# Performance work log

Hardware: AMD Instinct MI355X
Metric: run time of the kernel (lower is better)

The kernel has to match this reference:

```python
import jax, jax.numpy as jnp
import numpy as np

N_NODES = 50000
N_EDGES = 800000
N_GRAPHS = 500
DIM = 64          # node feature dim
NG = 64           # num gaussians (edge rbf dim)
CUTOFF = 12.0
NCONV = 3
HID = 128
NTYPES = 100      # atom vocabulary for embedding
EPS = 1e-5        # batchnorm eps


def _bn(x, g, b):
    # training-mode batchnorm over the leading (edge/node) axis
    m = jnp.mean(x, axis=0)
    v = jnp.var(x, axis=0)
    return g * (x - m) * jax.lax.rsqrt(v + EPS) + b


def setup_inputs() -> dict:
    key = jax.random.key(0)
    ks = jax.random.split(key, 12)
    atom_types = jax.random.randint(ks[0], (N_NODES,), 0, NTYPES)
    src = jax.random.randint(ks[1], (N_EDGES,), 0, N_NODES)
    dst = jax.random.randint(ks[2], (N_EDGES,), 0, N_NODES)
    graph_ids = jnp.sort(jax.random.randint(ks[3], (N_NODES,), 0, N_GRAPHS))
    distance = jax.random.uniform(ks[4], (N_EDGES,), dtype=jnp.float32) * CUTOFF
    cin = 2 * DIM + NG
    s = 0.05
    embed_table = jax.random.normal(ks[5], (NTYPES, DIM), dtype=jnp.float32) * s
    W1 = jax.random.normal(ks[6], (NCONV, cin, DIM), dtype=jnp.float32) * s
    b1 = jnp.zeros((NCONV, DIM), jnp.float32)
    W2 = jax.random.normal(ks[7], (NCONV, cin, DIM), dtype=jnp.float32) * s
    b2 = jnp.zeros((NCONV, DIM), jnp.float32)
    g1 = jnp.ones((NCONV, DIM), jnp.float32); bt1 = jnp.zeros((NCONV, DIM), jnp.float32)
    g2 = jnp.ones((NCONV, DIM), jnp.float32); bt2 = jnp.zeros((NCONV, DIM), jnp.float32)
    g3 = jnp.ones((NCONV, DIM), jnp.float32); bt3 = jnp.zeros((NCONV, DIM), jnp.float32)
    Wfc = jax.random.normal(ks[8], (DIM, HID), dtype=jnp.float32) * s
    bfc = jnp.zeros((HID,), jnp.float32)
    Wout = jax.random.normal(ks[9], (HID, 1), dtype=jnp.float32) * s
    bout = jnp.zeros((1,), jnp.float32)
    return dict(atom_types=atom_types, src=src, dst=dst, graph_ids=graph_ids,
                distance=distance, embed_table=embed_table,
                W1=W1, b1=b1, W2=W2, b2=b2,
                g1=g1, bt1=bt1, g2=g2, bt2=bt2, g3=g3, bt3=bt3,
                Wfc=Wfc, bfc=bfc, Wout=Wout, bout=bout)


def reference(atom_types, src, dst, graph_ids, distance, embed_table,
              W1, b1, W2, b2, g1, bt1, g2, bt2, g3, bt3,
              Wfc, bfc, Wout, bout):
    # embedding lookup
    node = embed_table[atom_types]                           # [N, DIM]
    # RBF expansion of distances (gaussian smearing on [0, CUTOFF])
    mu = jnp.linspace(0.0, CUTOFF, NG, dtype=jnp.float32)
    coeff = -0.5 / (mu[1] - mu[0]) ** 2
    rbf = jnp.exp(coeff * (distance[:, None] - mu) ** 2)      # [E, NG]

    for i in range(NCONV):
        # gather: concat(src feats, dst feats, edge rbf)
        te = jnp.concatenate([node[src], node[dst], rbf], axis=-1)  # [E, 192]
        nbr_filter = jax.nn.sigmoid(_bn(te @ W1[i] + b1[i], g1[i], bt1[i]))
        # NOTE: faithful to the source bug: bn2 is applied to nbr_filter,
        # so fc_full2 (W2/b2) output is computed in torch but unused.
        nbr_core = jax.nn.softplus(_bn(nbr_filter, g2[i], bt2[i]))
        h = nbr_filter * nbr_core                              # [E, DIM]
        # scatter-sum messages to destination nodes
        agg = jax.ops.segment_sum(h, dst, num_segments=N_NODES)
        node = node + _bn(agg, g3[i], bt3[i])

    # avg pooling per graph
    sums = jax.ops.segment_sum(node, graph_ids, num_segments=N_GRAPHS)
    cnts = jax.ops.segment_sum(jnp.ones((N_NODES, 1), node.dtype), graph_ids,
                               num_segments=N_GRAPHS)
    crys = sums / jnp.maximum(cnts, 1.0)                       # [G, DIM]

    crys = jax.nn.softplus(crys) @ Wfc + bfc
    crys = jax.nn.softplus(crys)
    return crys @ Wout + bout                                  # [G, 1]
```

## Files before the change

kernel.cpp:

```cpp
#include <hip/hip_runtime.h>
#include <hip/hip_fp16.h>
#include <math.h>

#define DIM 64
#define NG 64
#define CIN 192
#define HID 128
#define NCONV 3
#define TB 2048
#define CUTOFF 12.0f
#define EPS 1e-5f
#define SCB 256

typedef int i2v __attribute__((ext_vector_type(2)));
typedef int i4v __attribute__((ext_vector_type(4)));

__device__ __forceinline__ float sp_(float y) {
    return fmaxf(y, 0.f) + __logf(1.f + __expf(-fabsf(y)));
}
__device__ __forceinline__ float sig_(float y) {
    return 1.f / (1.f + __expf(-y));
}
__device__ __forceinline__ float2 h2f2_bits(int bits) {
    __half2 h;
    __builtin_memcpy(&h, &bits, 4);
    return __half22float2(h);
}
__device__ __forceinline__ int f2h2_bits(float a, float b) {
    __half2 h;
    h.x = __float2half(a);
    h.y = __float2half(b);
    int r;
    __builtin_memcpy(&r, &h, 4);
    return r;
}

__global__ void k_tables(const float* __restrict__ W1, __half2* __restrict__ Tp) {
    int row = blockIdx.x;
    int l = row / TB, i = row % TB;
    int d = threadIdx.x;
    const float stepmu = CUTOFF / (float)(NG - 1);
    const float coeff = -0.5f / (stepmu * stepmu);
    const float stepx = CUTOFF / (float)(TB - 1);
    float x0 = (float)i * stepx;
    float x1 = fminf((float)(i + 1), (float)(TB - 1)) * stepx;
    __shared__ float r0[NG];
    __shared__ float r1[NG];
    float mu = (float)d * stepmu;
    float d0 = x0 - mu, d1 = x1 - mu;
    r0[d] = expf(coeff * d0 * d0);
    r1[d] = expf(coeff * d1 * d1);
    __syncthreads();
    const float* w = W1 + (size_t)(l * CIN + 2 * DIM) * DIM;
    float a0 = 0.f, a1 = 0.f;
#pragma unroll 8
    for (int g = 0; g < NG; ++g) {
        float wv = w[g * DIM + d];
        a0 += r0[g] * wv;
        a1 += r1[g] * wv;
    }
    __half2 hh;
    hh.x = __float2half(a0);
    hh.y = __float2half(a1);
    Tp[(size_t)row * DIM + d] = hh;
}

__global__ void k_hist(const int* __restrict__ dst, int* __restrict__ cnt, int E) {
    for (int e = blockIdx.x * blockDim.x + threadIdx.x; e < E;
         e += gridDim.x * blockDim.x)
        atomicAdd(&cnt[dst[e]], 1);
}

__global__ void k_scanA(const int* __restrict__ cnt, int* __restrict__ bsum, int N) {
    __shared__ int lds[SCB];
    int i = blockIdx.x * SCB + threadIdx.x;
    lds[threadIdx.x] = (i < N) ? cnt[i] : 0;
    __syncthreads();
    for (int o = SCB / 2; o > 0; o >>= 1) {
        if (threadIdx.x < o) lds[threadIdx.x] += lds[threadIdx.x + o];
        __syncthreads();
    }
    if (threadIdx.x == 0) bsum[blockIdx.x] = lds[0];
}

__global__ void k_scanB(const int* __restrict__ bsum, int* __restrict__ bexcl, int NB) {
    __shared__ int lds[SCB];
    int t = threadIdx.x;
    int v = (t < NB) ? bsum[t] : 0;
    lds[t] = v;
    __syncthreads();
    for (int o = 1; o < SCB; o <<= 1) {
        int add = (t >= o) ? lds[t - o] : 0;
        __syncthreads();
        lds[t] += add;
        __syncthreads();
    }
    if (t < NB) bexcl[t] = lds[t] - v;
}

__global__ void k_scanC(const int* __restrict__ cnt, const int* __restrict__ bexcl,
                        int* __restrict__ off, int* __restrict__ cursor, int N, int E) {
    __shared__ int lds[SCB];
    int t = threadIdx.x;
    int i = blockIdx.x * SCB + t;
    int v = (i < N) ? cnt[i] : 0;
    lds[t] = v;
    __syncthreads();
    for (int o = 1; o < SCB; o <<= 1) {
        int add = (t >= o) ? lds[t - o] : 0;
        __syncthreads();
        lds[t] += add;
        __syncthreads();
    }
    if (i < N) {
        int excl = bexcl[blockIdx.x] + lds[t] - v;
        off[i] = excl;
        cursor[i] = excl;
        if (i == N - 1) off[N] = E;
    }
}

__global__ void k_scatter(const int* __restrict__ src, const int* __restrict__ dst,
                          const float* __restrict__ dist, int* __restrict__ cursor,
                          int2* __restrict__ es, int E) {
    const float inv_step = (float)(TB - 1) / CUTOFF;
    for (int e = blockIdx.x * blockDim.x + threadIdx.x; e < E;
         e += gridDim.x * blockDim.x) {
        int t = dst[e];
        int pos = atomicAdd(&cursor[t], 1);
        es[pos] = make_int2(src[e], __float_as_int(dist[e] * inv_step));
    }
}

template <int FIRST>
__global__ void __launch_bounds__(256) k_pq(
        const int* __restrict__ at, const float* __restrict__ emb,
        float* __restrict__ node, const float* __restrict__ agg,
        const double* __restrict__ st, const float* __restrict__ g3,
        const float* __restrict__ bt3, double invN,
        const float* __restrict__ W1, const float* __restrict__ b1, int l,
        __half* __restrict__ P16, float* __restrict__ Q, int N) {
    __shared__ float wa[DIM * DIM];
    __shared__ float wb[DIM * DIM];
    const float* WA = W1 + (size_t)(l * CIN) * DIM;
    for (int k = threadIdx.x; k < DIM * DIM; k += blockDim.x) {
        wa[k] = WA[k];
        wb[k] = WA[DIM * DIM + k];
    }
    int lane = threadIdx.x & 63, w = threadIdx.x >> 6;
    float bv = b1[lane];
    float a3 = 0.f, c3 = 0.f;
    if (!FIRST) {
        double m = st[lane] * invN;
        double v = st[64 + lane] * invN - m * m;
        a3 = g3[lane] / sqrtf((float)v + EPS);
        c3 = bt3[lane] - a3 * (float)m;
    }
    __syncthreads();
    int wpb = blockDim.x >> 6;
    for (int n = blockIdx.x * wpb + w; n < N; n += gridDim.x * wpb) {
        float nv;
        if (FIRST) {
            nv = emb[at[n] * DIM + lane];
        } else {
            nv = node[n * DIM + lane] + a3 * agg[n * DIM + lane] + c3;
        }
        node[n * DIM + lane] = nv;
        float ap = 0.f, aq = bv;
#pragma unroll 8
        for (int k = 0; k < DIM; ++k) {
            float b = __shfl(nv, k);
            ap += b * wa[k * DIM + lane];
            aq += b * wb[k * DIM + lane];
        }
        P16[n * DIM + lane] = __float2half(ap);
        Q[n * DIM + lane] = aq;
    }
}

__global__ void __launch_bounds__(256) k_convA(
        const int* __restrict__ off, const int2* __restrict__ es,
        const __half* __restrict__ P16, const float* __restrict__ Q,
        const __half2* __restrict__ Tp,
        double* __restrict__ stats, __half* __restrict__ z16, int N) {
    int lane = threadIdx.x & 63;
    int w = threadIdx.x >> 6;
    int dg = lane & 15;
    int slot = lane >> 4;
    int d0 = dg * 4;
    float s00 = 0.f, s01 = 0.f, s02 = 0.f, s03 = 0.f;
    float s10 = 0.f, s11 = 0.f, s12 = 0.f, s13 = 0.f;
    int gw = blockIdx.x * 4 + w, nw = gridDim.x * 4;
    for (int n = gw; n < N; n += nw) {
        int e0 = off[n], e1 = off[n + 1];
        if (e0 >= e1) continue;
        float4 q4 = *(const float4*)(Q + (size_t)n * DIM + d0);
        for (int eb = e0; eb < e1; eb += 8) {
            int eA = eb + slot, eB = eA + 4;
            bool vA = (eA < e1), vB = (eB < e1);
            int2 evA = es[vA ? eA : e1 - 1];
            int2 evB = es[vB ? eB : e1 - 1];
            float uA = __int_as_float(evA.y), uB = __int_as_float(evB.y);
            int iA = (int)uA, iB = (int)uB;
            iA = max(0, min(iA, TB - 2));
            iB = max(0, min(iB, TB - 2));
            float frA = uA - (float)iA, frB = uB - (float)iB;
            i2v pbA = *(const i2v*)(P16 + (size_t)evA.x * DIM + d0);
            i2v pbB = *(const i2v*)(P16 + (size_t)evB.x * DIM + d0);
            i4v tbA = *(const i4v*)(Tp + (size_t)iA * DIM + d0);
            i4v tbB = *(const i4v*)(Tp + (size_t)iB * DIM + d0);
            {
                float2 p01 = h2f2_bits(pbA.x), p23 = h2f2_bits(pbA.y);
                float2 t0 = h2f2_bits(tbA.x), t1 = h2f2_bits(tbA.y);
                float2 t2 = h2f2_bits(tbA.z), t3 = h2f2_bits(tbA.w);
                float z0 = p01.x + t0.x + frA * (t0.y - t0.x) + q4.x;
                float z1 = p01.y + t1.x + frA * (t1.y - t1.x) + q4.y;
                float z2 = p23.x + t2.x + frA * (t2.y - t2.x) + q4.z;
                float z3 = p23.y + t3.x + frA * (t3.y - t3.x) + q4.w;
                if (vA) {
                    i2v zz;
                    zz.x = f2h2_bits(z0, z1);
                    zz.y = f2h2_bits(z2, z3);
                    *(i2v*)(z16 + (size_t)eA * DIM + d0) = zz;
                    s00 += z0; s10 += z0 * z0;
                    s01 += z1; s11 += z1 * z1;
                    s02 += z2; s12 += z2 * z2;
                    s03 += z3; s13 += z3 * z3;
                }
            }
            {
                float2 p01 = h2f2_bits(pbB.x), p23 = h2f2_bits(pbB.y);
                float2 t0 = h2f2_bits(tbB.x), t1 = h2f2_bits(tbB.y);
                float2 t2 = h2f2_bits(tbB.z), t3 = h2f2_bits(tbB.w);
                float z0 = p01.x + t0.x + frB * (t0.y - t0.x) + q4.x;
                float z1 = p01.y + t1.x + frB * (t1.y - t1.x) + q4.y;
                float z2 = p23.x + t2.x + frB * (t2.y - t2.x) + q4.z;
                float z3 = p23.y + t3.x + frB * (t3.y - t3.x) + q4.w;
                if (vB) {
                    i2v zz;
                    zz.x = f2h2_bits(z0, z1);
                    zz.y = f2h2_bits(z2, z3);
                    *(i2v*)(z16 + (size_t)eB * DIM + d0) = zz;
                    s00 += z0; s10 += z0 * z0;
                    s01 += z1; s11 += z1 * z1;
                    s02 += z2; s12 += z2 * z2;
                    s03 += z3; s13 += z3 * z3;
                }
            }
        }
    }
    __shared__ float r0[4][64][4];
    __shared__ float r1[4][64][4];
    r0[w][lane][0] = s00; r0[w][lane][1] = s01;
    r0[w][lane][2] = s02; r0[w][lane][3] = s03;
    r1[w][lane][0] = s10; r1[w][lane][1] = s11;
    r1[w][lane][2] = s12; r1[w][lane][3] = s13;
    __syncthreads();
    if (threadIdx.x < 64) {
        int d = threadIdx.x;
        int dgg = d >> 2, q = d & 3;
        float t0 = 0.f, t1 = 0.f;
#pragma unroll
        for (int ww = 0; ww < 4; ++ww)
#pragma unroll
            for (int sl = 0; sl < 4; ++sl) {
                t0 += r0[ww][sl * 16 + dgg][q];
                t1 += r1[ww][sl * 16 + dgg][q];
            }
        atomicAdd(&stats[d], (double)t0);
        atomicAdd(&stats[64 + d], (double)t1);
    }
}

__global__ void __launch_bounds__(256) k_statsF(
        __half* __restrict__ zf16,
        const double* __restrict__ stA, const float* __restrict__ gA,
        const float* __restrict__ btA,
        double* __restrict__ stats, int total8, double invE) {
    int gq = threadIdx.x & 7;
    float a1[8], c1[8];
#pragma unroll
    for (int q = 0; q < 8; ++q) {
        int d = gq * 8 + q;
        double m = stA[d] * invE;
        double v = stA[64 + d] * invE - m * m;
        a1[q] = gA[d] / sqrtf((float)v + EPS);
        c1[q] = btA[d] - a1[q] * (float)m;
    }
    float s0[8] = {0, 0, 0, 0, 0, 0, 0, 0};
    float s1[8] = {0, 0, 0, 0, 0, 0, 0, 0};
    i4v* z4 = (i4v*)zf16;
    int tid = blockIdx.x * blockDim.x + threadIdx.x;
    int stride = gridDim.x * blockDim.x;
    for (int i = tid; i < total8; i += stride) {
        i4v v = z4[i];
        float2 p0 = h2f2_bits(v.x);
        float2 p1 = h2f2_bits(v.y);
        float2 p2 = h2f2_bits(v.z);
        float2 p3 = h2f2_bits(v.w);
        float f0 = sig_(a1[0] * p0.x + c1[0]);
        float f1 = sig_(a1[1] * p0.y + c1[1]);
        float f2 = sig_(a1[2] * p1.x + c1[2]);
        float f3 = sig_(a1[3] * p1.y + c1[3]);
        float f4 = sig_(a1[4] * p2.x + c1[4]);
        float f5 = sig_(a1[5] * p2.y + c1[5]);
        float f6 = sig_(a1[6] * p3.x + c1[6]);
        float f7 = sig_(a1[7] * p3.y + c1[7]);
        i4v o;
        o.x = f2h2_bits(f0, f1);
        o.y = f2h2_bits(f2, f3);
        o.z = f2h2_bits(f4, f5);
        o.w = f2h2_bits(f6, f7);
        z4[i] = o;
        s0[0] += f0; s1[0] += f0 * f0;
        s0[1] += f1; s1[1] += f1 * f1;
        s0[2] += f2; s1[2] += f2 * f2;
        s0[3] += f3; s1[3] += f3 * f3;
        s0[4] += f4; s1[4] += f4 * f4;
        s0[5] += f5; s1[5] += f5 * f5;
        s0[6] += f6; s1[6] += f6 * f6;
        s0[7] += f7; s1[7] += f7 * f7;
    }
    __shared__ float lds[256][16];
#pragma unroll
    for (int q = 0; q < 8; ++q) {
        lds[threadIdx.x][q] = s0[q];
        lds[threadIdx.x][8 + q] = s1[q];
    }
    __syncthreads();
    if (threadIdx.x < 64) {
        int d = threadIdx.x;
        int grp = d >> 3, j = d & 7;
        float t0 = 0.f, t1 = 0.f;
        for (int k = 0; k < 32; ++k) {
            int t = k * 8 + grp;
            t0 += lds[t][j];
            t1 += lds[t][8 + j];
        }
        atomicAdd(&stats[d], (double)t0);
        atomicAdd(&stats[64 + d], (double)t1);
    }
}

__global__ void __launch_bounds__(256) k_aggF(
        const int* __restrict__ off, const __half* __restrict__ f16,
        const double* __restrict__ stB, const float* __restrict__ gB,
        const float* __restrict__ btB,
        double* __restrict__ stats, float* __restrict__ agg, int N, double invE) {
    int lane = threadIdx.x & 63;
    int w = threadIdx.x >> 6;
    int dg = lane & 7;
    int slot = lane >> 3;
    int d0 = dg * 8;
    float a2[8], c2[8];
#pragma unroll
    for (int q = 0; q < 8; ++q) {
        int d = d0 + q;
        double m = stB[d] * invE, v = stB[64 + d] * invE - m * m;
        a2[q] = gB[d] / sqrtf((float)v + EPS);
        c2[q] = btB[d] - a2[q] * (float)m;
    }
    float s0[8] = {0, 0, 0, 0, 0, 0, 0, 0};
    float s1[8] = {0, 0, 0, 0, 0, 0, 0, 0};
    int gw = blockIdx.x * 4 + w, nw = gridDim.x * 4;
    for (int n = gw; n < N; n += nw) {
        int e0 = off[n], e1 = off[n + 1];
        float tot[8] = {0, 0, 0, 0, 0, 0, 0, 0};
        for (int eb = e0; eb < e1; eb += 16) {
            int eA = eb + slot, eB = eA + 8;
            float mkA = (eA < e1) ? 1.f : 0.f;
            float mkB = (eB < e1) ? 1.f : 0.f;
            int ecA = (eA < e1) ? eA : (e1 - 1);
            int ecB = (eB < e1) ? eB : (e1 - 1);
            i4v zbA = *(const i4v*)(f16 + (size_t)ecA * DIM + d0);
            i4v zbB = *(const i4v*)(f16 + (size_t)ecB * DIM + d0);
            float2 a0 = h2f2_bits(zbA.x), a1v = h2f2_bits(zbA.y);
            float2 a2v = h2f2_bits(zbA.z), a3v = h2f2_bits(zbA.w);
            float2 b0 = h2f2_bits(zbB.x), b1v = h2f2_bits(zbB.y);
            float2 b2v = h2f2_bits(zbB.z), b3v = h2f2_bits(zbB.w);
            float fA[8] = {a0.x, a0.y, a1v.x, a1v.y, a2v.x, a2v.y, a3v.x, a3v.y};
            float fB[8] = {b0.x, b0.y, b1v.x, b1v.y, b2v.x, b2v.y, b3v.x, b3v.y};
#pragma unroll
            for (int q = 0; q < 8; ++q) {
                float hA = fA[q] * sp_(a2[q] * fA[q] + c2[q]);
                float hB = fB[q] * sp_(a2[q] * fB[q] + c2[q]);
                tot[q] += mkA * hA + mkB * hB;
            }
        }
#pragma unroll
        for (int q = 0; q < 8; ++q) {
            float v = tot[q];
            v += __shfl_xor(v, 8);
            v += __shfl_xor(v, 16);
            v += __shfl_xor(v, 32);
            tot[q] = v;
        }
        if (slot == 0) {
            float4 w0 = make_float4(tot[0], tot[1], tot[2], tot[3]);
            float4 w1 = make_float4(tot[4], tot[5], tot[6], tot[7]);
            *(float4*)(agg + (size_t)n * DIM + d0) = w0;
            *(float4*)(agg + (size_t)n * DIM + d0 + 4) = w1;
#pragma unroll
            for (int q = 0; q < 8; ++q) {
                s0[q] += tot[q];
                s1[q] += tot[q] * tot[q];
            }
        }
    }
    __shared__ float r0[4][8][8];
    __shared__ float r1[4][8][8];
    if (slot == 0) {
#pragma unroll
        for (int q = 0; q < 8; ++q) {
            r0[w][dg][q] = s0[q];
            r1[w][dg][q] = s1[q];
        }
    }
    __syncthreads();
    if (threadIdx.x < 64) {
        int d = threadIdx.x;
        int dgg = d >> 3, q = d & 7;
        float t0 = 0.f, t1 = 0.f;
#pragma unroll
        for (int ww = 0; ww < 4; ++ww) {
            t0 += r0[ww][dgg][q];
            t1 += r1[ww][dgg][q];
        }
        atomicAdd(&stats[d], (double)t0);
        atomicAdd(&stats[64 + d], (double)t1);
    }
}

template <int MODE>
__global__ void __launch_bounds__(256) k_conv(
        const int* __restrict__ off, const int2* __restrict__ es,
        const __half* __restrict__ P16, const float* __restrict__ Q,
        const __half2* __restrict__ Tp,
        const double* __restrict__ stA, const float* __restrict__ gA,
        const float* __restrict__ btA,
        const double* __restrict__ stB, const float* __restrict__ gB,
        const float* __restrict__ btB,
        double* __restrict__ stats, float* __restrict__ agg, int N, double invE) {
    int lane = threadIdx.x & 63;
    int w = threadIdx.x >> 6;
    float a1 = 0.f, c1 = 0.f, a2 = 0.f, c2 = 0.f;
    if (MODE >= 2) {
        double m = stA[lane] * invE;
        double v = stA[64 + lane] * invE - m * m;
        a1 = gA[lane] / sqrtf((float)v + EPS);
        c1 = btA[lane] - a1 * (float)m;
    }
    if (MODE == 3) {
        double m = stB[lane] * invE;
        double v = stB[64 + lane] * invE - m * m;
        a2 = gB[lane] / sqrtf((float)v + EPS);
        c2 = btB[lane] - a2 * (float)m;
    }
    float s0 = 0.f, s1 = 0.f;
    int gw = blockIdx.x * 4 + w, nw = gridDim.x * 4;
    for (int n = gw; n < N; n += nw) {
        int e0 = off[n], e1 = off[n + 1];
        float qc = Q[n * DIM + lane];
        float acc = 0.f;
        auto body = [&](int2 ev) {
            float u = __int_as_float(ev.y);
            int i = (int)u;
            i = max(0, min(i, TB - 2));
            float fr = u - (float)i;
            float2 t2 = __half22float2(Tp[(size_t)i * DIM + lane]);
            float p = __half2float(P16[(size_t)ev.x * DIM + lane]);
            float z = p + t2.x + fr * (t2.y - t2.x) + qc;
            if (MODE == 0) { s0 += z; s1 += z * z; }
            else {
                float f = sig_(a1 * z + c1);
                if (MODE == 2) { s0 += f; s1 += f * f; }
                else acc += f * sp_(a2 * f + c2);
            }
        };
        int e = e0;
        for (; e + 2 <= e1; e += 2) { body(es[e]); body(es[e + 1]); }
        if (e < e1) body(es[e]);
        if (MODE == 3) {
            agg[n * DIM + lane] = acc;
            s0 += acc; s1 += acc * acc;
        }
    }
    __shared__ float r0[4][64];
    __shared__ float r1[4][64];
    r0[w][lane] = s0;
    r1[w][lane] = s1;
    __syncthreads();
    if (threadIdx.x < 64) {
        int d = threadIdx.x;
        float t0 = r0[0][d] + r0[1][d] + r0[2][d] + r0[3][d];
        float t1 = r1[0][d] + r1[1][d] + r1[2][d] + r1[3][d];
        atomicAdd(&stats[d], (double)t0);
        atomicAdd(&stats[64 + d], (double)t1);
    }
}

__global__ void k_head(const float* __restrict__ node, const float* __restrict__ agg,
                       const double* __restrict__ st, const float* __restrict__ g3,
                       const float* __restrict__ bt3, double invN,
                       const int* __restrict__ gid, int N,
                       const float* __restrict__ Wfc, const float* __restrict__ bfc,
                       const float* __restrict__ Wout, const float* __restrict__ bout,
                       float* __restrict__ out) {
    int g = blockIdx.x;
    __shared__ int bounds[2];
    if (threadIdx.x == 0) {
        int lo = 0, hi = N;
        while (lo < hi) { int mid = (lo + hi) >> 1; if (gid[mid] < g) lo = mid + 1; else hi = mid; }
        bounds[0] = lo;
        int lo2 = lo; hi = N;
        while (lo2 < hi) { int mid = (lo2 + hi) >> 1; if (gid[mid] < g + 1) lo2 = mid + 1; else hi = mid; }
        bounds[1] = lo2;
    }
    __syncthreads();
    int s = bounds[0], e = bounds[1];
    __shared__ float sp[DIM];
    if (threadIdx.x < DIM) {
        int d = threadIdx.x;
        double mm = st[d] * invN;
        double vv = st[64 + d] * invN - mm * mm;
        float a3 = g3[d] / sqrtf((float)vv + EPS);
        float c3 = bt3[d] - a3 * (float)mm;
        float sn = 0.f, sa = 0.f;
        for (int n = s; n < e; ++n) {
            sn += node[(size_t)n * DIM + d];
            sa += agg[(size_t)n * DIM + d];
        }
        float cntf = (float)max(e - s, 1);
        float m = (sn + a3 * sa) / cntf + c3;
        sp[d] = (m > 0.f) ? m + log1pf(expf(-m)) : log1pf(expf(m));
    }
    __syncthreads();
    int j = threadIdx.x;
    float hj = bfc[j];
#pragma unroll 8
    for (int k = 0; k < DIM; ++k) hj += sp[k] * Wfc[k * HID + j];
    hj = (hj > 0.f) ? hj + log1pf(expf(-hj)) : log1pf(expf(hj));
    __shared__ float red[HID];
    red[j] = hj * Wout[j];
    __syncthreads();
    for (int o = HID / 2; o > 0; o >>= 1) {
        if (j < o) red[j] += red[j + o];
        __syncthreads();
    }
    if (j == 0) out[g] = red[0] + bout[0];
}

extern "C" void kernel_launch(void* const* d_in, const int* in_sizes, int n_in,
                              void* d_out, int out_size, void* d_ws, size_t ws_size,
                              hipStream_t stream) {
    const int* atom_types = (const int*)d_in[0];
    const int* src = (const int*)d_in[1];
    const int* dst = (const int*)d_in[2];
    const int* gid = (const int*)d_in[3];
    const float* dist = (const float*)d_in[4];
    const float* emb = (const float*)d_in[5];
    const float* W1 = (const float*)d_in[6];
    const float* b1 = (const float*)d_in[7];
    const float* g1 = (const float*)d_in[10];
    const float* bt1 = (const float*)d_in[11];
    const float* g2 = (const float*)d_in[12];
    const float* bt2 = (const float*)d_in[13];
    const float* g3 = (const float*)d_in[14];
    const float* bt3 = (const float*)d_in[15];
    const float* Wfc = (const float*)d_in[16];
    const float* bfc = (const float*)d_in[17];
    const float* Wout = (const float*)d_in[18];
    const float* bout = (const float*)d_in[19];

    int N = in_sizes[0];
    int E = in_sizes[1];
    int G = out_size;
    int NB = (N + SCB - 1) / SCB;

    char* ws = (char*)d_ws;
    auto alloc = [&](size_t bytes) -> char* {
        char* p = ws;
        ws += (bytes + 255) & ~(size_t)255;
        return p;
    };
    size_t nd = (size_t)N * DIM * sizeof(float);
    float* node = (float*)alloc(nd);
    __half* P16 = (__half*)alloc(nd / 2);
    float* Q = (float*)alloc(nd);
    float* agg = (float*)alloc(nd);
    __half2* Tp = (__half2*)alloc((size_t)NCONV * TB * DIM * sizeof(__half2));
    double* stats = (double*)alloc((size_t)NCONV * 3 * 128 * sizeof(double));
    int* off = (int*)alloc((size_t)(N + 1) * sizeof(int));
    int* cursor = (int*)alloc((size_t)N * sizeof(int));
    int* cnt = (int*)alloc((size_t)N * sizeof(int));
    int* bsum = (int*)alloc(SCB * sizeof(int));
    int* bexcl = (int*)alloc(SCB * sizeof(int));
    int2* es = (int2*)alloc((size_t)E * sizeof(int2));
    size_t zbytes = (size_t)E * DIM * sizeof(__half);
    size_t used = (size_t)(ws - (char*)d_ws);
    bool planZ = (used + zbytes) <= ws_size;
    __half* z16 = planZ ? (__half*)alloc(zbytes) : nullptr;

    hipMemsetAsync(stats, 0, (size_t)NCONV * 3 * 128 * sizeof(double), stream);
    hipMemsetAsync(cnt, 0, (size_t)N * sizeof(int), stream);

    k_tables<<<NCONV * TB, 64, 0, stream>>>(W1, Tp);

    k_hist<<<1024, 256, 0, stream>>>(dst, cnt, E);
    k_scanA<<<NB, SCB, 0, stream>>>(cnt, bsum, N);
    k_scanB<<<1, SCB, 0, stream>>>(bsum, bexcl, NB);
    k_scanC<<<NB, SCB, 0, stream>>>(cnt, bexcl, off, cursor, N, E);
    k_scatter<<<1024, 256, 0, stream>>>(src, dst, dist, cursor, es, E);

    double invE = 1.0 / (double)E;
    double invN = 1.0 / (double)N;

    for (int l = 0; l < NCONV; ++l) {
        const __half2* Tl = Tp + (size_t)l * TB * DIM;
        double* st1 = stats + (size_t)(l * 3 + 0) * 128;
        double* st2 = stats + (size_t)(l * 3 + 1) * 128;
        double* st3 = stats + (size_t)(l * 3 + 2) * 128;

        if (l == 0) {
            k_pq<1><<<2048, 256, 0, stream>>>(atom_types, emb, node, nullptr,
                                              nullptr, nullptr, nullptr, 0.0,
                                              W1, b1 + l * DIM, l, P16, Q, N);
        } else {
            double* st3p = stats + (size_t)((l - 1) * 3 + 2) * 128;
            k_pq<0><<<2048, 256, 0, stream>>>(atom_types, emb, node, agg,
                                              st3p, g3 + (l - 1) * DIM,
                                              bt3 + (l - 1) * DIM, invN,
                                              W1, b1 + l * DIM, l, P16, Q, N);
        }

        if (planZ) {
            k_convA<<<2048, 256, 0, stream>>>(off, es, P16, Q, Tl, st1, z16, N);
            k_statsF<<<2048, 256, 0, stream>>>(z16, st1, g1 + l * DIM, bt1 + l * DIM,
                                               st2, E * 8, invE);
            k_aggF<<<2048, 256, 0, stream>>>(off, z16,
                                             st2, g2 + l * DIM, bt2 + l * DIM,
                                             st3, agg, N, invE);
        } else {
            k_conv<0><<<2048, 256, 0, stream>>>(off, es, P16, Q, Tl,
                                                nullptr, nullptr, nullptr,
                                                nullptr, nullptr, nullptr,
                                                st1, nullptr, N, invE);
            k_conv<2><<<2048, 256, 0, stream>>>(off, es, P16, Q, Tl,
                                                st1, g1 + l * DIM, bt1 + l * DIM,
                                                nullptr, nullptr, nullptr,
                                                st2, nullptr, N, invE);
            k_conv<3><<<2048, 256, 0, stream>>>(off, es, P16, Q, Tl,
                                                st1, g1 + l * DIM, bt1 + l * DIM,
                                                st2, g2 + l * DIM, bt2 + l * DIM,
                                                st3, agg, N, invE);
        }
    }

    double* st3f = stats + (size_t)(2 * 3 + 2) * 128;
    k_head<<<G, HID, 0, stream>>>(node, agg, st3f, g3 + 2 * DIM, bt3 + 2 * DIM,
                                  invN, gid, N, Wfc, bfc, Wout, bout, (float*)d_out);
}
```

Measured before the change: 971.8 us.

## Fuse per-layer conv kernels and head into one cooperative persistent kernel

Replaces the sequence of 13 per-layer launches (pq, convA, statsF, aggF for each layer, plus head) with a single cooperative kernel that separates the phases with grid-wide syncs. The aim is to remove launch gaps and per-launch setup. The trade-off is a grid capped by occupancy, so each block handles more work per phase, plus the cost of grid.sync barriers. The non-Z fallback path k_conv is removed, and the multi-kernel path is kept only as a fallback when the cooperative launch fails.

```diff
diff --git a/kernel.cpp b/kernel.cpp
--- a/kernel.cpp
+++ b/kernel.cpp
@@ -1,6 +1,9 @@
 #include <hip/hip_runtime.h>
+#include <hip/hip_cooperative_groups.h>
 #include <hip/hip_fp16.h>
 #include <math.h>
+
+namespace cg = cooperative_groups;
 
 #define DIM 64
 #define NG 64
@@ -160,11 +163,8 @@
     int wpb = blockDim.x >> 6;
     for (int n = blockIdx.x * wpb + w; n < N; n += gridDim.x * wpb) {
         float nv;
-        if (FIRST) {
-            nv = emb[at[n] * DIM + lane];
-        } else {
-            nv = node[n * DIM + lane] + a3 * agg[n * DIM + lane] + c3;
-        }
+        if (FIRST) nv = emb[at[n] * DIM + lane];
+        else nv = node[n * DIM + lane] + a3 * agg[n * DIM + lane] + c3;
         node[n * DIM + lane] = nv;
         float ap = 0.f, aq = bv;
 #pragma unroll 8
@@ -185,8 +185,7 @@
         double* __restrict__ stats, __half* __restrict__ z16, int N) {
     int lane = threadIdx.x & 63;
     int w = threadIdx.x >> 6;
-    int dg = lane & 15;
-    int slot = lane >> 4;
+    int dg = lane & 15, slot = lane >> 4;
     int d0 = dg * 4;
     float s00 = 0.f, s01 = 0.f, s02 = 0.f, s03 = 0.f;
     float s10 = 0.f, s11 = 0.f, s12 = 0.f, s13 = 0.f;
@@ -349,8 +348,7 @@
         double* __restrict__ stats, float* __restrict__ agg, int N, double invE) {
     int lane = threadIdx.x & 63;
     int w = threadIdx.x >> 6;
-    int dg = lane & 7;
-    int slot = lane >> 3;
+    int dg = lane & 7, slot = lane >> 3;
     int d0 = dg * 8;
     float a2[8], c2[8];
 #pragma unroll
@@ -431,74 +429,6 @@
     }
 }
 
-template <int MODE>
-__global__ void __launch_bounds__(256) k_conv(
-        const int* __restrict__ off, const int2* __restrict__ es,
-        const __half* __restrict__ P16, const float* __restrict__ Q,
-        const __half2* __restrict__ Tp,
-        const double* __restrict__ stA, const float* __restrict__ gA,
-        const float* __restrict__ btA,
-        const double* __restrict__ stB, const float* __restrict__ gB,
-        const float* __restrict__ btB,
-        double* __restrict__ stats, float* __restrict__ agg, int N, double invE) {
-    int lane = threadIdx.x & 63;
-    int w = threadIdx.x >> 6;
-    float a1 = 0.f, c1 = 0.f, a2 = 0.f, c2 = 0.f;
-    if (MODE >= 2) {
-        double m = stA[lane] * invE;
-        double v = stA[64 + lane] * invE - m * m;
-        a1 = gA[lane] / sqrtf((float)v + EPS);
-        c1 = btA[lane] - a1 * (float)m;
-    }
-    if (MODE == 3) {
-        double m = stB[lane] * invE;
-        double v = stB[64 + lane] * invE - m * m;
-        a2 = gB[lane] / sqrtf((float)v + EPS);
-        c2 = btB[lane] - a2 * (float)m;
-    }
-    float s0 = 0.f, s1 = 0.f;
-    int gw = blockIdx.x * 4 + w, nw = gridDim.x * 4;
-    for (int n = gw; n < N; n += nw) {
-        int e0 = off[n], e1 = off[n + 1];
-        float qc = Q[n * DIM + lane];
-        float acc = 0.f;
-        auto body = [&](int2 ev) {
-            float u = __int_as_float(ev.y);
-            int i = (int)u;
-            i = max(0, min(i, TB - 2));
-            float fr = u - (float)i;
-            float2 t2 = __half22float2(Tp[(size_t)i * DIM + lane]);
-            float p = __half2float(P16[(size_t)ev.x * DIM + lane]);
-            float z = p + t2.x + fr * (t2.y - t2.x) + qc;
-            if (MODE == 0) { s0 += z; s1 += z * z; }
-            else {
-                float f = sig_(a1 * z + c1);
-                if (MODE == 2) { s0 += f; s1 += f * f; }
-                else acc += f * sp_(a2 * f + c2);
-            }
-        };
-        int e = e0;
-        for (; e + 2 <= e1; e += 2) { body(es[e]); body(es[e + 1]); }
-        if (e < e1) body(es[e]);
-        if (MODE == 3) {
-            agg[n * DIM + lane] = acc;
-            s0 += acc; s1 += acc * acc;
-        }
-    }
-    __shared__ float r0[4][64];
-    __shared__ float r1[4][64];
-    r0[w][lane] = s0;
-    r1[w][lane] = s1;
-    __syncthreads();
-    if (threadIdx.x < 64) {
-        int d = threadIdx.x;
-        float t0 = r0[0][d] + r0[1][d] + r0[2][d] + r0[3][d];
-        float t1 = r1[0][d] + r1[1][d] + r1[2][d] + r1[3][d];
-        atomicAdd(&stats[d], (double)t0);
-        atomicAdd(&stats[64 + d], (double)t1);
-    }
-}
-
 __global__ void k_head(const float* __restrict__ node, const float* __restrict__ agg,
                        const double* __restrict__ st, const float* __restrict__ g3,
                        const float* __restrict__ bt3, double invN,
@@ -548,6 +478,366 @@
         __syncthreads();
     }
     if (j == 0) out[g] = red[0] + bout[0];
+}
+
+struct MegaArgs {
+    const int* at; const float* emb;
+    float* node; __half* P16; float* Q; float* agg;
+    const __half2* Tp; const int* off; const int2* es;
+    __half* z16;
+    const float* W1; const float* b1;
+    const float* g1; const float* bt1;
+    const float* g2; const float* bt2;
+    const float* g3; const float* bt3;
+    double* stats;
+    const int* gid;
+    const float* Wfc; const float* bfc; const float* Wout; const float* bout;
+    float* out;
+    int N, E, G;
+    double invE, invN;
+};
+
+__global__ void __launch_bounds__(256, 4) k_mega(MegaArgs a) {
+    cg::grid_group grid = cg::this_grid();
+    __shared__ __align__(16) char smem[32768];
+    int lane = threadIdx.x & 63;
+    int w = threadIdx.x >> 6;
+
+    for (int l = 0; l < NCONV; ++l) {
+        double* st1 = a.stats + (size_t)(l * 3 + 0) * 128;
+        double* st2 = a.stats + (size_t)(l * 3 + 1) * 128;
+        double* st3 = a.stats + (size_t)(l * 3 + 2) * 128;
+        const __half2* Tl = a.Tp + (size_t)l * TB * DIM;
+
+        {
+            float* wa = (float*)smem;
+            float* wb = (float*)(smem + 16384);
+            const float* WA = a.W1 + (size_t)(l * CIN) * DIM;
+            for (int k = threadIdx.x; k < DIM * DIM; k += blockDim.x) {
+                wa[k] = WA[k];
+                wb[k] = WA[DIM * DIM + k];
+            }
+            float bv = a.b1[l * DIM + lane];
+            float a3 = 0.f, c3 = 0.f;
+            if (l > 0) {
+                const double* stp = a.stats + (size_t)((l - 1) * 3 + 2) * 128;
+                double m = stp[lane] * a.invN;
+                double v = stp[64 + lane] * a.invN - m * m;
+                a3 = a.g3[(l - 1) * DIM + lane] / sqrtf((float)v + EPS);
+                c3 = a.bt3[(l - 1) * DIM + lane] - a3 * (float)m;
+            }
+            __syncthreads();
+            int wpb = blockDim.x >> 6;
+            for (int n = blockIdx.x * wpb + w; n < a.N; n += gridDim.x * wpb) {
+                float nv;
+                if (l == 0) nv = a.emb[a.at[n] * DIM + lane];
+                else nv = a.node[n * DIM + lane] + a3 * a.agg[n * DIM + lane] + c3;
+                a.node[n * DIM + lane] = nv;
+                float ap = 0.f, aq = bv;
+#pragma unroll 8
+                for (int k = 0; k < DIM; ++k) {
+                    float b = __shfl(nv, k);
+                    ap += b * wa[k * DIM + lane];
+                    aq += b * wb[k * DIM + lane];
+                }
+                a.P16[n * DIM + lane] = __float2half(ap);
+                a.Q[n * DIM + lane] = aq;
+            }
+        }
+        grid.sync();
+
+        {
+            int dg = lane & 15, slot = lane >> 4;
+            int d0 = dg * 4;
+            float s00 = 0.f, s01 = 0.f, s02 = 0.f, s03 = 0.f;
+            float s10 = 0.f, s11 = 0.f, s12 = 0.f, s13 = 0.f;
+            int gw = blockIdx.x * 4 + w, nw = gridDim.x * 4;
+            for (int n = gw; n < a.N; n += nw) {
+                int e0 = a.off[n], e1 = a.off[n + 1];
+                if (e0 >= e1) continue;
+                float4 q4 = *(const float4*)(a.Q + (size_t)n * DIM + d0);
+                for (int eb = e0; eb < e1; eb += 8) {
+                    int eA = eb + slot, eB = eA + 4;
+                    bool vA = (eA < e1), vB = (eB < e1);
+                    int2 evA = a.es[vA ? eA : e1 - 1];
+                    int2 evB = a.es[vB ? eB : e1 - 1];
+                    float uA = __int_as_float(evA.y), uB = __int_as_float(evB.y);
+                    int iA = (int)uA, iB = (int)uB;
+                    iA = max(0, min(iA, TB - 2));
+                    iB = max(0, min(iB, TB - 2));
+                    float frA = uA - (float)iA, frB = uB - (float)iB;
+                    i2v pbA = *(const i2v*)(a.P16 + (size_t)evA.x * DIM + d0);
+                    i2v pbB = *(const i2v*)(a.P16 + (size_t)evB.x * DIM + d0);
+                    i4v tbA = *(const i4v*)(Tl + (size_t)iA * DIM + d0);
+                    i4v tbB = *(const i4v*)(Tl + (size_t)iB * DIM + d0);
+                    {
+                        float2 p01 = h2f2_bits(pbA.x), p23 = h2f2_bits(pbA.y);
+                        float2 t0 = h2f2_bits(tbA.x), t1 = h2f2_bits(tbA.y);
+                        float2 t2 = h2f2_bits(tbA.z), t3 = h2f2_bits(tbA.w);
+                        float z0 = p01.x + t0.x + frA * (t0.y - t0.x) + q4.x;
+                        float z1 = p01.y + t1.x + frA * (t1.y - t1.x) + q4.y;
+                        float z2 = p23.x + t2.x + frA * (t2.y - t2.x) + q4.z;
+                        float z3 = p23.y + t3.x + frA * (t3.y - t3.x) + q4.w;
+                        if (vA) {
+                            i2v zz;
+                            zz.x = f2h2_bits(z0, z1);
+                            zz.y = f2h2_bits(z2, z3);
+                            *(i2v*)(a.z16 + (size_t)eA * DIM + d0) = zz;
+                            s00 += z0; s10 += z0 * z0;
+                            s01 += z1; s11 += z1 * z1;
+                            s02 += z2; s12 += z2 * z2;
+                            s03 += z3; s13 += z3 * z3;
+                        }
+                    }
+                    {
+                        float2 p01 = h2f2_bits(pbB.x), p23 = h2f2_bits(pbB.y);
+                        float2 t0 = h2f2_bits(tbB.x), t1 = h2f2_bits(tbB.y);
+                        float2 t2 = h2f2_bits(tbB.z), t3 = h2f2_bits(tbB.w);
+                        float z0 = p01.x + t0.x + frB * (t0.y - t0.x) + q4.x;
+                        float z1 = p01.y + t1.x + frB * (t1.y - t1.x) + q4.y;
+                        float z2 = p23.x + t2.x + frB * (t2.y - t2.x) + q4.z;
+                        float z3 = p23.y + t3.x + frB * (t3.y - t3.x) + q4.w;
+                        if (vB) {
+                            i2v zz;
+                            zz.x = f2h2_bits(z0, z1);
+                            zz.y = f2h2_bits(z2, z3);
+                            *(i2v*)(a.z16 + (size_t)eB * DIM + d0) = zz;
+                            s00 += z0; s10 += z0 * z0;
+                            s01 += z1; s11 += z1 * z1;
+                            s02 += z2; s12 += z2 * z2;
+                            s03 += z3; s13 += z3 * z3;
+                        }
+                    }
+                }
+            }
+            float (*r0)[64][4] = (float(*)[64][4])smem;
+            float (*r1)[64][4] = (float(*)[64][4])(smem + 4096);
+            __syncthreads();
+            r0[w][lane][0] = s00; r0[w][lane][1] = s01;
+            r0[w][lane][2] = s02; r0[w][lane][3] = s03;
+            r1[w][lane][0] = s10; r1[w][lane][1] = s11;
+            r1[w][lane][2] = s12; r1[w][lane][3] = s13;
+            __syncthreads();
+            if (threadIdx.x < 64) {
+                int d = threadIdx.x;
+                int dgg = d >> 2, q = d & 3;
+                float t0 = 0.f, t1 = 0.f;
+#pragma unroll
+                for (int ww = 0; ww < 4; ++ww)
+#pragma unroll
+                    for (int sl = 0; sl < 4; ++sl) {
+                        t0 += r0[ww][sl * 16 + dgg][q];
+                        t1 += r1[ww][sl * 16 + dgg][q];
+                    }
+                atomicAdd(&st1[d], (double)t0);
+                atomicAdd(&st1[64 + d], (double)t1);
+            }
+        }
+        grid.sync();
+
+        {
+            int gq = threadIdx.x & 7;
+            float a1[8], c1[8];
+#pragma unroll
+            for (int q = 0; q < 8; ++q) {
+                int d = gq * 8 + q;
+                double m = st1[d] * a.invE;
+                double v = st1[64 + d] * a.invE - m * m;
+                a1[q] = a.g1[l * DIM + d] / sqrtf((float)v + EPS);
+                c1[q] = a.bt1[l * DIM + d] - a1[q] * (float)m;
+            }
+            float s0[8] = {0, 0, 0, 0, 0, 0, 0, 0};
+            float s1[8] = {0, 0, 0, 0, 0, 0, 0, 0};
+            i4v* z4 = (i4v*)a.z16;
+            int total8 = a.E * 8;
+            int tid = blockIdx.x * blockDim.x + threadIdx.x;
+            int stride = gridDim.x * blockDim.x;
+            for (int i = tid; i < total8; i += stride) {
+                i4v v = z4[i];
+                float2 p0 = h2f2_bits(v.x);
+                float2 p1 = h2f2_bits(v.y);
+                float2 p2 = h2f2_bits(v.z);
+                float2 p3 = h2f2_bits(v.w);
+                float f0 = sig_(a1[0] * p0.x + c1[0]);
+                float f1 = sig_(a1[1] * p0.y + c1[1]);
+                float f2 = sig_(a1[2] * p1.x + c1[2]);
+                float f3 = sig_(a1[3] * p1.y + c1[3]);
+                float f4 = sig_(a1[4] * p2.x + c1[4]);
+                float f5 = sig_(a1[5] * p2.y + c1[5]);
+                float f6 = sig_(a1[6] * p3.x + c1[6]);
+                float f7 = sig_(a1[7] * p3.y + c1[7]);
+                i4v o;
+                o.x = f2h2_bits(f0, f1);
+                o.y = f2h2_bits(f2, f3);
+                o.z = f2h2_bits(f4, f5);
+                o.w = f2h2_bits(f6, f7);
+                z4[i] = o;
+                s0[0] += f0; s1[0] += f0 * f0;
+                s0[1] += f1; s1[1] += f1 * f1;
+                s0[2] += f2; s1[2] += f2 * f2;
+                s0[3] += f3; s1[3] += f3 * f3;
+                s0[4] += f4; s1[4] += f4 * f4;
+                s0[5] += f5; s1[5] += f5 * f5;
+                s0[6] += f6; s1[6] += f6 * f6;
+                s0[7] += f7; s1[7] += f7 * f7;
+            }
+            float (*lds)[16] = (float(*)[16])smem;
+            __syncthreads();
+#pragma unroll
+            for (int q = 0; q < 8; ++q) {
+                lds[threadIdx.x][q] = s0[q];
+                lds[threadIdx.x][8 + q] = s1[q];
+            }
+            __syncthreads();
+            if (threadIdx.x < 64) {
+                int d = threadIdx.x;
+                int grp = d >> 3, j = d & 7;
+                float t0 = 0.f, t1 = 0.f;
+                for (int k = 0; k < 32; ++k) {
+                    int t = k * 8 + grp;
+                    t0 += lds[t][j];
+                    t1 += lds[t][8 + j];
+                }
+                atomicAdd(&st2[d], (double)t0);
+                atomicAdd(&st2[64 + d], (double)t1);
+            }
+        }
+        grid.sync();
+
+        {
+            int dg = lane & 7, slot = lane >> 3;
+            int d0 = dg * 8;
+            float a2[8], c2[8];
+#pragma unroll
+            for (int q = 0; q < 8; ++q) {
+                int d = d0 + q;
+                double m = st2[d] * a.invE, v = st2[64 + d] * a.invE - m * m;
+                a2[q] = a.g2[l * DIM + d] / sqrtf((float)v + EPS);
+                c2[q] = a.bt2[l * DIM + d] - a2[q] * (float)m;
+            }
+            float s0[8] = {0, 0, 0, 0, 0, 0, 0, 0};
+            float s1[8] = {0, 0, 0, 0, 0, 0, 0, 0};
+            int gw = blockIdx.x * 4 + w, nw = gridDim.x * 4;
+            for (int n = gw; n < a.N; n += nw) {
+                int e0 = a.off[n], e1 = a.off[n + 1];
+                float tot[8] = {0, 0, 0, 0, 0, 0, 0, 0};
+                for (int eb = e0; eb < e1; eb += 16) {
+                    int eA = eb + slot, eB = eA + 8;
+                    float mkA = (eA < e1) ? 1.f : 0.f;
+                    float mkB = (eB < e1) ? 1.f : 0.f;
+                    int ecA = (eA < e1) ? eA : (e1 - 1);
+                    int ecB = (eB < e1) ? eB : (e1 - 1);
+                    i4v zbA = *(const i4v*)(a.z16 + (size_t)ecA * DIM + d0);
+                    i4v zbB = *(const i4v*)(a.z16 + (size_t)ecB * DIM + d0);
+                    float2 a0 = h2f2_bits(zbA.x), a1v = h2f2_bits(zbA.y);
+                    float2 a2v = h2f2_bits(zbA.z), a3v = h2f2_bits(zbA.w);
+                    float2 b0 = h2f2_bits(zbB.x), b1v = h2f2_bits(zbB.y);
+                    float2 b2v = h2f2_bits(zbB.z), b3v = h2f2_bits(zbB.w);
+                    float fA[8] = {a0.x, a0.y, a1v.x, a1v.y, a2v.x, a2v.y, a3v.x, a3v.y};
+                    float fB[8] = {b0.x, b0.y, b1v.x, b1v.y, b2v.x, b2v.y, b3v.x, b3v.y};
+#pragma unroll
+                    for (int q = 0; q < 8; ++q) {
+                        float hA = fA[q] * sp_(a2[q] * fA[q] + c2[q]);
+                        float hB = fB[q] * sp_(a2[q] * fB[q] + c2[q]);
+                        tot[q] += mkA * hA + mkB * hB;
+                    }
+                }
+#pragma unroll
+                for (int q = 0; q < 8; ++q) {
+                    float v = tot[q];
+                    v += __shfl_xor(v, 8);
+                    v += __shfl_xor(v, 16);
+                    v += __shfl_xor(v, 32);
+                    tot[q] = v;
+                }
+                if (slot == 0) {
+                    float4 w0 = make_float4(tot[0], tot[1], tot[2], tot[3]);
+                    float4 w1 = make_float4(tot[4], tot[5], tot[6], tot[7]);
+                    *(float4*)(a.agg + (size_t)n * DIM + d0) = w0;
+                    *(float4*)(a.agg + (size_t)n * DIM + d0 + 4) = w1;
+#pragma unroll
+                    for (int q = 0; q < 8; ++q) {
+                        s0[q] += tot[q];
+                        s1[q] += tot[q] * tot[q];
+                    }
+                }
+            }
+            float (*r0)[8][8] = (float(*)[8][8])smem;
+            float (*r1)[8][8] = (float(*)[8][8])(smem + 1024);
+            __syncthreads();
+            if (slot == 0) {
+#pragma unroll
+                for (int q = 0; q < 8; ++q) {
+                    r0[w][dg][q] = s0[q];
+                    r1[w][dg][q] = s1[q];
+                }
+            }
+            __syncthreads();
+            if (threadIdx.x < 64) {
+                int d = threadIdx.x;
+                int dgg = d >> 3, q = d & 7;
+                float t0 = 0.f, t1 = 0.f;
+#pragma unroll
+                for (int ww = 0; ww < 4; ++ww) {
+                    t0 += r0[ww][dgg][q];
+                    t1 += r1[ww][dgg][q];
+                }
+                atomicAdd(&st3[d], (double)t0);
+                atomicAdd(&st3[64 + d], (double)t1);
+            }
+        }
+        grid.sync();
+    }
+
+    {
+        const double* st = a.stats + (size_t)(2 * 3 + 2) * 128;
+        int* bounds = (int*)smem;
+        float* sp = (float*)(smem + 16);
+        float* red = (float*)(smem + 16 + DIM * 4);
+        for (int g = blockIdx.x; g < a.G; g += gridDim.x) {
+            if (threadIdx.x == 0) {
+                int lo = 0, hi = a.N;
+                while (lo < hi) { int mid = (lo + hi) >> 1; if (a.gid[mid] < g) lo = mid + 1; else hi = mid; }
+                bounds[0] = lo;
+                int lo2 = lo; hi = a.N;
+                while (lo2 < hi) { int mid = (lo2 + hi) >> 1; if (a.gid[mid] < g + 1) lo2 = mid + 1; else hi = mid; }
+                bounds[1] = lo2;
+            }
+            __syncthreads();
+            int s = bounds[0], e = bounds[1];
+            if (threadIdx.x < DIM) {
+                int d = threadIdx.x;
+                double mm = st[d] * a.invN;
+                double vv = st[64 + d] * a.invN - mm * mm;
+                float a3 = a.g3[2 * DIM + d] / sqrtf((float)vv + EPS);
+                float c3 = a.bt3[2 * DIM + d] - a3 * (float)mm;
+                float sn = 0.f, sa = 0.f;
+                for (int n = s; n < e; ++n) {
+                    sn += a.node[(size_t)n * DIM + d];
+                    sa += a.agg[(size_t)n * DIM + d];
+                }
+                float cntf = (float)max(e - s, 1);
+                float m = (sn + a3 * sa) / cntf + c3;
+                sp[d] = (m > 0.f) ? m + log1pf(expf(-m)) : log1pf(expf(m));
+            }
+            __syncthreads();
+            int j = threadIdx.x;
+            if (j < HID) {
+                float hj = a.bfc[j];
+#pragma unroll 8
+                for (int k = 0; k < DIM; ++k) hj += sp[k] * a.Wfc[k * HID + j];
+                hj = (hj > 0.f) ? hj + log1pf(expf(-hj)) : log1pf(expf(hj));
+                red[j] = hj * a.Wout[j];
+            }
+            __syncthreads();
+            for (int o = HID / 2; o > 0; o >>= 1) {
+                if (j < o) red[j] += red[j + o];
+                __syncthreads();
+            }
+            if (j == 0) a.out[g] = red[0] + a.bout[0];
+            __syncthreads();
+        }
+    }
 }
 
 extern "C" void kernel_launch(void* const* d_in, const int* in_sizes, int n_in,
@@ -605,7 +895,6 @@
     hipMemsetAsync(cnt, 0, (size_t)N * sizeof(int), stream);
 
     k_tables<<<NCONV * TB, 64, 0, stream>>>(W1, Tp);
-
     k_hist<<<1024, 256, 0, stream>>>(dst, cnt, E);
     k_scanA<<<NB, SCB, 0, stream>>>(cnt, bsum, N);
     k_scanB<<<1, SCB, 0, stream>>>(bsum, bexcl, NB);
@@ -615,48 +904,60 @@
     double invE = 1.0 / (double)E;
     double invN = 1.0 / (double)N;
 
-    for (int l = 0; l < NCONV; ++l) {
-        const __half2* Tl = Tp + (size_t)l * TB * DIM;
-        double* st1 = stats + (size_t)(l * 3 + 0) * 128;
-        double* st2 = stats + (size_t)(l * 3 + 1) * 128;
-        double* st3 = stats + (size_t)(l * 3 + 2) * 128;
-
-        if (l == 0) {
-            k_pq<1><<<2048, 256, 0, stream>>>(atom_types, emb, node, nullptr,
-                                              nullptr, nullptr, nullptr, 0.0,
-                                              W1, b1 + l * DIM, l, P16, Q, N);
-        } else {
-            double* st3p = stats + (size_t)((l - 1) * 3 + 2) * 128;
-            k_pq<0><<<2048, 256, 0, stream>>>(atom_types, emb, node, agg,
-                                              st3p, g3 + (l - 1) * DIM,
-                                              bt3 + (l - 1) * DIM, invN,
-                                              W1, b1 + l * DIM, l, P16, Q, N);
-        }
-
-        if (planZ) {
+    bool megaDone = false;
+    if (planZ) {
+        int maxPerCU = 0, numCU = 0, dev = 0;
+        hipGetDevice(&dev);
+        hipDeviceGetAttribute(&numCU, hipDeviceAttributeMultiprocessorCount, dev);
+        hipOccupancyMaxActiveBlocksPerMultiprocessor(&maxPerCU, (const void*)k_mega, 256, 0);
+        long long maxBlocks = (long long)maxPerCU * (long long)numCU;
+        if (maxBlocks > 0) {
+            int grid = (int)((maxBlocks > 2048) ? 2048 : maxBlocks);
+            MegaArgs ma;
+            ma.at = atom_types; ma.emb = emb;
+            ma.node = node; ma.P16 = P16; ma.Q = Q; ma.agg = agg;
+            ma.Tp = Tp; ma.off = off; ma.es = es; ma.z16 = z16;
+            ma.W1 = W1; ma.b1 = b1;
+            ma.g1 = g1; ma.bt1 = bt1; ma.g2 = g2; ma.bt2 = bt2;
+            ma.g3 = g3; ma.bt3 = bt3;
+            ma.stats = stats; ma.gid = gid;
+            ma.Wfc = Wfc; ma.bfc = bfc; ma.Wout = Wout; ma.bout = bout;
+            ma.out = (float*)d_out;
+            ma.N = N; ma.E = E; ma.G = G;
+            ma.invE = invE; ma.invN = invN;
+            void* kargs[] = { (void*)&ma };
+            hipError_t err = hipLaunchCooperativeKernel((void*)k_mega, dim3(grid),
+                                                        dim3(256), kargs, 0, stream);
+            megaDone = (err == hipSuccess);
+        }
+    }
+
+    if (!megaDone) {
+        for (int l = 0; l < NCONV; ++l) {
+            const __half2* Tl = Tp + (size_t)l * TB * DIM;
+            double* st1 = stats + (size_t)(l * 3 + 0) * 128;
+            double* st2 = stats + (size_t)(l * 3 + 1) * 128;
+            double* st3 = stats + (size_t)(l * 3 + 2) * 128;
+            if (l == 0) {
+                k_pq<1><<<2048, 256, 0, stream>>>(atom_types, emb, node, nullptr,
+                                                  nullptr, nullptr, nullptr, 0.0,
+                                                  W1, b1 + l * DIM, l, P16, Q, N);
+            } else {
+                double* st3p = stats + (size_t)((l - 1) * 3 + 2) * 128;
+                k_pq<0><<<2048, 256, 0, stream>>>(atom_types, emb, node, agg,
+                                                  st3p, g3 + (l - 1) * DIM,
+                                                  bt3 + (l - 1) * DIM, invN,
+                                                  W1, b1 + l * DIM, l, P16, Q, N);
+            }
             k_convA<<<2048, 256, 0, stream>>>(off, es, P16, Q, Tl, st1, z16, N);
             k_statsF<<<2048, 256, 0, stream>>>(z16, st1, g1 + l * DIM, bt1 + l * DIM,
                                                st2, E * 8, invE);
             k_aggF<<<2048, 256, 0, stream>>>(off, z16,
                                              st2, g2 + l * DIM, bt2 + l * DIM,
                                              st3, agg, N, invE);
-        } else {
-            k_conv<0><<<2048, 256, 0, stream>>>(off, es, P16, Q, Tl,
-                                                nullptr, nullptr, nullptr,
-                                                nullptr, nullptr, nullptr,
-                                                st1, nullptr, N, invE);
-            k_conv<2><<<2048, 256, 0, stream>>>(off, es, P16, Q, Tl,
-                                                st1, g1 + l * DIM, bt1 + l * DIM,
-                                                nullptr, nullptr, nullptr,
-                                                st2, nullptr, N, invE);
-            k_conv<3><<<2048, 256, 0, stream>>>(off, es, P16, Q, Tl,
-                                                st1, g1 + l * DIM, bt1 + l * DIM,
-                                                st2, g2 + l * DIM, bt2 + l * DIM,
-                                                st3, agg, N, invE);
-        }
-    }
-
-    double* st3f = stats + (size_t)(2 * 3 + 2) * 128;
-    k_head<<<G, HID, 0, stream>>>(node, agg, st3f, g3 + 2 * DIM, bt3 + 2 * DIM,
-                                  invN, gid, N, Wfc, bfc, Wout, bout, (float*)d_out);
-}
+        }
+        double* st3f = stats + (size_t)(2 * 3 + 2) * 128;
+        k_head<<<G, HID, 0, stream>>>(node, agg, st3f, g3 + 2 * DIM, bt3 + 2 * DIM,
+                                      invN, gid, N, Wfc, bfc, Wout, bout, (float*)d_out);
+    }
+}
```

Result: slower. 1.653 ms (+70.1%).
